# Kernel optimization log

Measured on AMD Instinct MI355X. Metric: run time of the kernel, lower is better.

The kernel has to match this reference:

```python
import jax, jax.numpy as jnp
import numpy as np
from jax import lax

B, T, D = 1024, 100, 12
NEG_SLOPE = 0.01  # torch.nn.LeakyReLU default


def setup_inputs() -> dict:
    key = jax.random.key(0)
    ks = jax.random.split(key, 6)
    y0 = jax.random.normal(ks[0], (B, T, D), dtype=jnp.float32)
    # shared, increasing time grid per row (forward only uses row 0, made relative)
    t = jnp.broadcast_to(jnp.linspace(0.0, 1.0, T, dtype=jnp.float32), (B, T)) + 0.0
    def lin(k, fan_in, fan_out):
        s = 1.0 / np.sqrt(fan_in)
        return jax.random.normal(k, (fan_in, fan_out), dtype=jnp.float32) * s
    W1 = lin(ks[1], D, 300); b1 = jnp.zeros((300,), jnp.float32)
    W2 = lin(ks[2], 300, 100); b2 = jnp.zeros((100,), jnp.float32)
    W3 = lin(ks[3], 100, 50); b3 = jnp.zeros((50,), jnp.float32)
    W4 = lin(ks[4], 50, D); b4 = jnp.zeros((D,), jnp.float32)
    return {"y0": y0, "t": t, "W1": W1, "b1": b1, "W2": W2, "b2": b2,
            "W3": W3, "b3": b3, "W4": W4, "b4": b4}


def _mlp(x, W1, b1, W2, b2, W3, b3, W4, b4):
    h = jax.nn.leaky_relu(x @ W1 + b1, NEG_SLOPE)
    h = jax.nn.leaky_relu(h @ W2 + b2, NEG_SLOPE)
    h = jax.nn.leaky_relu(h @ W3 + b3, NEG_SLOPE)
    return h @ W4 + b4


def reference(y0, t, W1, b1, W2, b2, W3, b3, W4, b4):
    # t_span: relative times of batch row 0 (as in the torch forward)
    t_rel = t[0] - t[0, 0]                       # [T]
    x0 = y0[:, 0, :]                             # [B, D] initial state
    f = lambda x: _mlp(x, W1, b1, W2, b2, W3, b3, W4, b4)

    def rk4_step(x, dt):
        k1 = f(x)
        k2 = f(x + 0.5 * dt * k1)
        k3 = f(x + 0.5 * dt * k2)
        k4 = f(x + dt * k3)
        x_new = x + (dt / 6.0) * (k1 + 2.0 * k2 + 2.0 * k3 + k4)
        return x_new, x_new

    dts = t_rel[1:] - t_rel[:-1]                 # [T-1]
    _, traj = lax.scan(rk4_step, x0, dts)        # [T-1, B, D]
    traj = jnp.concatenate([x0[None], traj], axis=0)  # [T, B, D]
    return jnp.swapaxes(traj, 0, 1)              # [B, T, D]
```

## Files before the change

kernel.cpp:

```cpp
#include <hip/hip_runtime.h>


typedef float v2f __attribute__((ext_vector_type(2)));
typedef float v4f __attribute__((ext_vector_type(4)));

constexpr int TT = 100;
constexpr int D  = 12;
constexpr int H1 = 300;
constexpr int H2 = 100;
constexpr int H3 = 50;
constexpr float NEG = 0.01f;

__device__ __forceinline__ float lrelu(float x) { return fmaxf(x, NEG * x); }
__device__ __forceinline__ v2f lo2(v4f v) { return __builtin_shufflevector(v, v, 0, 1); }
__device__ __forceinline__ v2f hi2(v4f v) { return __builtin_shufflevector(v, v, 2, 3); }
__device__ __forceinline__ v2f pkfma(v2f a, v2f b, v2f c) {
#if __has_builtin(__builtin_elementwise_fma)
    return __builtin_elementwise_fma(a, b, c);
#else
    return a * b + c;
#endif
}

__global__ __launch_bounds__(512)
void node_rk4_kernel(const float* __restrict__ y0, const float* __restrict__ t,
                     const float* __restrict__ W1, const float* __restrict__ b1,
                     const float* __restrict__ W2, const float* __restrict__ b2,
                     const float* __restrict__ W3, const float* __restrict__ b3,
                     const float* __restrict__ W4, const float* __restrict__ b4,
                     float* __restrict__ out)
{
    __shared__ __align__(16) float sW1 [D * H1];
    __shared__ __align__(16) float sW3c[25 * 200];
    __shared__ __align__(16) float sW4 [52 * 12];
    __shared__ __align__(16) float h1T [304 * 4];
    __shared__ __align__(16) float pL2 [32 * 104];
    __shared__ __align__(16) float h2e [4 * 104];
    __shared__ __align__(16) float h3e [4 * 52];
    __shared__ __align__(16) float sx  [48];
    __shared__ __align__(16) float sxe [48];
    __shared__ __align__(16) float sks [48];
    __shared__ float st [100];

    const int tid = threadIdx.x;
    const int l   = tid & 63;
    const int w   = tid >> 6;
    const bool l2act = (l < 50);

    const bool l1act = (tid < H1);
    const float rb1 = l1act ? b1[tid] : 0.0f;

    float w2a[38], w2b[38];
#pragma unroll
    for (int i = 0; i < 38; ++i) {
        const int k = w * 38 + i;
        float va = 0.0f, vb = 0.0f;
        if (l2act && k < H1) { va = W2[k * H2 + l]; vb = W2[k * H2 + l + 50]; }
        w2a[i] = va; w2b[i] = vb;
    }

    float rb2a = 0.f, rb2b = 0.f, rb3 = 0.f;
    if (w < 4 && l2act) { rb2a = b2[l]; rb2b = b2[l + 50]; rb3 = b3[l]; }

    const int u4 = tid - 256;
    const bool l4act = (u4 >= 0 && u4 < 192);
    int e4 = 0, j4 = 0, kq4 = 0;
    float b4v = 0.0f;
    if (l4act) {
        e4 = u4 / 48; const int r = u4 - e4 * 48; j4 = r >> 2; kq4 = r & 3;
        b4v = b4[j4];
    }

    for (int i = tid; i < D * H1; i += 512) sW1[i] = W1[i];
    for (int i = tid; i < H2 * H3; i += 512) {
        const int k = i / H3, j = i - k * H3;
        sW3c[(k >> 2) * 200 + j * 4 + (k & 3)] = W3[i];
    }
    for (int i = tid; i < 52 * 12; i += 512) sW4[i] = (i < H3 * D) ? W4[i] : 0.0f;
    if (tid < TT) st[tid] = t[tid];
    if (tid >= 104 && tid < 120) h1T[300 * 4 + (tid - 104)] = 0.0f;
    if (tid >= 120 && tid < 128) {
        const int u = tid - 120;
        h3e[(u >> 1) * 52 + 50 + (u & 1)] = 0.0f;
    }
    if (tid < 48) {
        const int e = tid / 12, j = tid - e * 12;
        const int g = (blockIdx.x * 4 + e) * (TT * D) + j;
        const float v = y0[g];
        sx[tid] = v;
        out[g]  = v;
    }
    __syncthreads();

    for (int s = 0; s < TT - 1; ++s) {
#pragma unroll 1
        for (int ev = 0; ev < 4; ++ev) {
            const float* xin = ev ? sxe : sx;

            if (l1act) {
                float wv[12];
#pragma unroll
                for (int k = 0; k < 12; ++k) wv[k] = sW1[k * H1 + tid];
                v4f r;
#pragma unroll
                for (int e = 0; e < 4; ++e) {
                    const v4f x0 = *(const v4f*)(xin + e * 12);
                    const v4f x1 = *(const v4f*)(xin + e * 12 + 4);
                    const v4f x2 = *(const v4f*)(xin + e * 12 + 8);
                    float a = rb1;
                    a = fmaf(x0.x, wv[0], a);  a = fmaf(x0.y, wv[1], a);
                    a = fmaf(x0.z, wv[2], a);  a = fmaf(x0.w, wv[3], a);
                    a = fmaf(x1.x, wv[4], a);  a = fmaf(x1.y, wv[5], a);
                    a = fmaf(x1.z, wv[6], a);  a = fmaf(x1.w, wv[7], a);
                    a = fmaf(x2.x, wv[8], a);  a = fmaf(x2.y, wv[9], a);
                    a = fmaf(x2.z, wv[10], a); a = fmaf(x2.w, wv[11], a);
                    r[e] = lrelu(a);
                }
                *(v4f*)(h1T + tid * 4) = r;
            }
            __syncthreads();

            {
                v2f a01A = {0,0}, a23A = {0,0}, a01B = {0,0}, a23B = {0,0};
                const float* hb = h1T + w * (38 * 4);
#pragma unroll
                for (int i = 0; i < 38; ++i) {
                    const v4f hv = *(const v4f*)(hb + i * 4);
                    const v2f wA = {w2a[i], w2a[i]};
                    const v2f wB = {w2b[i], w2b[i]};
                    a01A = pkfma(lo2(hv), wA, a01A);
                    a23A = pkfma(hi2(hv), wA, a23A);
                    a01B = pkfma(lo2(hv), wB, a01B);
                    a23B = pkfma(hi2(hv), wB, a23B);
                }
                if (l2act) {
                    pL2[(w * 4 + 0) * 104 + l]      = a01A.x;
                    pL2[(w * 4 + 1) * 104 + l]      = a01A.y;
                    pL2[(w * 4 + 2) * 104 + l]      = a23A.x;
                    pL2[(w * 4 + 3) * 104 + l]      = a23A.y;
                    pL2[(w * 4 + 0) * 104 + l + 50] = a01B.x;
                    pL2[(w * 4 + 1) * 104 + l + 50] = a01B.y;
                    pL2[(w * 4 + 2) * 104 + l + 50] = a23B.x;
                    pL2[(w * 4 + 3) * 104 + l + 50] = a23B.y;
                }
            }
            __syncthreads();

            if (w < 4 && l2act) {
                const int e = w;
                float va = rb2a, vb = rb2b;
#pragma unroll
                for (int q = 0; q < 8; ++q) {
                    va += pL2[(q * 4 + e) * 104 + l];
                    vb += pL2[(q * 4 + e) * 104 + l + 50];
                }
                h2e[e * 104 + l]      = lrelu(va);
                h2e[e * 104 + l + 50] = lrelu(vb);
                v2f acc = {0, 0};
                const float* hb2 = h2e + e * 104;
                const float* wb  = sW3c + l * 4;
#pragma unroll
                for (int c = 0; c < 25; ++c) {
                    const v4f wv = *(const v4f*)(wb + c * 200);
                    const v4f hv = *(const v4f*)(hb2 + c * 4);
                    acc = pkfma(lo2(hv), lo2(wv), acc);
                    acc = pkfma(hi2(hv), hi2(wv), acc);
                }
                h3e[e * 52 + l] = lrelu(acc.x + acc.y + rb3);
            }
            __syncthreads();

            if (l4act) {
                const int kb = kq4 * 13;
                float a = 0.0f;
                const float* hb3 = h3e + e4 * 52 + kb;
#pragma unroll
                for (int i = 0; i < 13; ++i)
                    a = fmaf(hb3[i], sW4[(kb + i) * 12 + j4], a);
                a += __shfl_xor(a, 1);
                a += __shfl_xor(a, 2);
                if (kq4 == 0) {
                    a += b4v;
                    const float dt = st[s + 1] - st[s];
                    const int bi = e4 * 12 + j4;
                    const float xc = sx[bi];
                    if (ev == 0)      { sks[bi] = a;        sxe[bi] = xc + 0.5f * dt * a; }
                    else if (ev == 1) { sks[bi] += 2.f * a; sxe[bi] = xc + 0.5f * dt * a; }
                    else if (ev == 2) { sks[bi] += 2.f * a; sxe[bi] = xc + dt * a; }
                    else {
                        const float xn = xc + dt * (1.0f / 6.0f) * (sks[bi] + a);
                        sx[bi] = xn;
                        out[(blockIdx.x * 4 + e4) * (TT * D) + (s + 1) * D + j4] = xn;
                    }
                }
            }
            __syncthreads();
        }
    }
}

extern "C" void kernel_launch(void* const* d_in, const int* in_sizes, int n_in,
                              void* d_out, int out_size, void* d_ws, size_t ws_size,
                              hipStream_t stream) {
    const float* y0 = (const float*)d_in[0];
    const float* t  = (const float*)d_in[1];
    const float* W1 = (const float*)d_in[2];
    const float* b1 = (const float*)d_in[3];
    const float* W2 = (const float*)d_in[4];
    const float* b2 = (const float*)d_in[5];
    const float* W3 = (const float*)d_in[6];
    const float* b3 = (const float*)d_in[7];
    const float* W4 = (const float*)d_in[8];
    const float* b4 = (const float*)d_in[9];
    float* out = (float*)d_out;

    node_rk4_kernel<<<256, 512, 0, stream>>>(y0, t, W1, b1, W2, b2, W3, b3, W4, b4, out);
}
```

Baseline: 1.170 ms.

## Fuse layers 3 and 4 per wave with readlane broadcasts, dropping a barrier

Layer 4 and the RK4 state update now run in the same four waves that compute layer 3, which removes one block-wide barrier per function evaluation. Layer 2 and layer 3 inputs are broadcast across lanes with readlane into scalar registers instead of being reread from LDS. The h2e buffer is gone. The RK4 state and accumulated slope live in registers rather than shared memory. In exchange there are many serial s_readlane instructions, with their latency and hazard stalls, and layers 3 and 4 are now serialised inside the same waves.

```diff
diff --git a/kernel.cpp b/kernel.cpp
--- a/kernel.cpp
+++ b/kernel.cpp
@@ -12,14 +12,8 @@
 constexpr float NEG = 0.01f;
 
 __device__ __forceinline__ float lrelu(float x) { return fmaxf(x, NEG * x); }
-__device__ __forceinline__ v2f lo2(v4f v) { return __builtin_shufflevector(v, v, 0, 1); }
-__device__ __forceinline__ v2f hi2(v4f v) { return __builtin_shufflevector(v, v, 2, 3); }
-__device__ __forceinline__ v2f pkfma(v2f a, v2f b, v2f c) {
-#if __has_builtin(__builtin_elementwise_fma)
-    return __builtin_elementwise_fma(a, b, c);
-#else
-    return a * b + c;
-#endif
+__device__ __forceinline__ float rdlane(float v, int lane) {
+    return __int_as_float(__builtin_amdgcn_readlane(__float_as_int(v), lane));
 }
 
 __global__ __launch_bounds__(512)
@@ -35,20 +29,16 @@
     __shared__ __align__(16) float sW4 [52 * 12];
     __shared__ __align__(16) float h1T [304 * 4];
     __shared__ __align__(16) float pL2 [32 * 104];
-    __shared__ __align__(16) float h2e [4 * 104];
     __shared__ __align__(16) float h3e [4 * 52];
     __shared__ __align__(16) float sx  [48];
     __shared__ __align__(16) float sxe [48];
-    __shared__ __align__(16) float sks [48];
     __shared__ float st [100];
 
     const int tid = threadIdx.x;
     const int l   = tid & 63;
     const int w   = tid >> 6;
     const bool l2act = (l < 50);
-
-    const bool l1act = (tid < H1);
-    const float rb1 = l1act ? b1[tid] : 0.0f;
+    const bool tw    = (w < 4);
 
     float w2a[38], w2b[38];
 #pragma unroll
@@ -59,17 +49,13 @@
         w2a[i] = va; w2b[i] = vb;
     }
 
+    const bool l1act = (tid < H1);
+    const float rb1 = l1act ? b1[tid] : 0.0f;
+
     float rb2a = 0.f, rb2b = 0.f, rb3 = 0.f;
-    if (w < 4 && l2act) { rb2a = b2[l]; rb2b = b2[l + 50]; rb3 = b3[l]; }
-
-    const int u4 = tid - 256;
-    const bool l4act = (u4 >= 0 && u4 < 192);
-    int e4 = 0, j4 = 0, kq4 = 0;
-    float b4v = 0.0f;
-    if (l4act) {
-        e4 = u4 / 48; const int r = u4 - e4 * 48; j4 = r >> 2; kq4 = r & 3;
-        b4v = b4[j4];
-    }
+    if (tw && l2act) { rb2a = b2[l]; rb2b = b2[l + 50]; rb3 = b3[l]; }
+    const int j4 = l >> 2, kq4 = l & 3;
+    const float b4v = (tw && l < 48) ? b4[j4] : 0.0f;
 
     for (int i = tid; i < D * H1; i += 512) sW1[i] = W1[i];
     for (int i = tid; i < H2 * H3; i += 512) {
@@ -92,7 +78,11 @@
     }
     __syncthreads();
 
+    float xreg = 0.0f, ks = 0.0f;
+    if (tw && l < 48 && kq4 == 0) xreg = sx[w * 12 + j4];
+
     for (int s = 0; s < TT - 1; ++s) {
+        const float dt = st[s + 1] - st[s];
 #pragma unroll 1
         for (int ev = 0; ev < 4; ++ev) {
             const float* xin = ev ? sxe : sx;
@@ -121,76 +111,79 @@
             __syncthreads();
 
             {
-                v2f a01A = {0,0}, a23A = {0,0}, a01B = {0,0}, a23B = {0,0};
-                const float* hb = h1T + w * (38 * 4);
+                const int ksrc = w * 38 + ((l < 38) ? l : 37);
+                const v4f hv = *(const v4f*)(h1T + ksrc * 4);
+                float a0A = 0.f, a0B = 0.f, a1A = 0.f, a1B = 0.f;
+                float a2A = 0.f, a2B = 0.f, a3A = 0.f, a3B = 0.f;
 #pragma unroll
                 for (int i = 0; i < 38; ++i) {
-                    const v4f hv = *(const v4f*)(hb + i * 4);
-                    const v2f wA = {w2a[i], w2a[i]};
-                    const v2f wB = {w2b[i], w2b[i]};
-                    a01A = pkfma(lo2(hv), wA, a01A);
-                    a23A = pkfma(hi2(hv), wA, a23A);
-                    a01B = pkfma(lo2(hv), wB, a01B);
-                    a23B = pkfma(hi2(hv), wB, a23B);
+                    const float h0 = rdlane(hv[0], i);
+                    const float h1 = rdlane(hv[1], i);
+                    const float h2 = rdlane(hv[2], i);
+                    const float h3 = rdlane(hv[3], i);
+                    a0A = fmaf(h0, w2a[i], a0A);  a0B = fmaf(h0, w2b[i], a0B);
+                    a1A = fmaf(h1, w2a[i], a1A);  a1B = fmaf(h1, w2b[i], a1B);
+                    a2A = fmaf(h2, w2a[i], a2A);  a2B = fmaf(h2, w2b[i], a2B);
+                    a3A = fmaf(h3, w2a[i], a3A);  a3B = fmaf(h3, w2b[i], a3B);
                 }
                 if (l2act) {
-                    pL2[(w * 4 + 0) * 104 + l]      = a01A.x;
-                    pL2[(w * 4 + 1) * 104 + l]      = a01A.y;
-                    pL2[(w * 4 + 2) * 104 + l]      = a23A.x;
-                    pL2[(w * 4 + 3) * 104 + l]      = a23A.y;
-                    pL2[(w * 4 + 0) * 104 + l + 50] = a01B.x;
-                    pL2[(w * 4 + 1) * 104 + l + 50] = a01B.y;
-                    pL2[(w * 4 + 2) * 104 + l + 50] = a23B.x;
-                    pL2[(w * 4 + 3) * 104 + l + 50] = a23B.y;
+                    pL2[(w * 4 + 0) * 104 + l]      = a0A;
+                    pL2[(w * 4 + 1) * 104 + l]      = a1A;
+                    pL2[(w * 4 + 2) * 104 + l]      = a2A;
+                    pL2[(w * 4 + 3) * 104 + l]      = a3A;
+                    pL2[(w * 4 + 0) * 104 + l + 50] = a0B;
+                    pL2[(w * 4 + 1) * 104 + l + 50] = a1B;
+                    pL2[(w * 4 + 2) * 104 + l + 50] = a2B;
+                    pL2[(w * 4 + 3) * 104 + l + 50] = a3B;
                 }
             }
             __syncthreads();
 
-            if (w < 4 && l2act) {
+            if (tw) {
                 const int e = w;
-                float va = rb2a, vb = rb2b;
-#pragma unroll
-                for (int q = 0; q < 8; ++q) {
-                    va += pL2[(q * 4 + e) * 104 + l];
-                    vb += pL2[(q * 4 + e) * 104 + l + 50];
-                }
-                h2e[e * 104 + l]      = lrelu(va);
-                h2e[e * 104 + l + 50] = lrelu(vb);
-                v2f acc = {0, 0};
-                const float* hb2 = h2e + e * 104;
-                const float* wb  = sW3c + l * 4;
-#pragma unroll
-                for (int c = 0; c < 25; ++c) {
-                    const v4f wv = *(const v4f*)(wb + c * 200);
-                    const v4f hv = *(const v4f*)(hb2 + c * 4);
-                    acc = pkfma(lo2(hv), lo2(wv), acc);
-                    acc = pkfma(hi2(hv), hi2(wv), acc);
-                }
-                h3e[e * 52 + l] = lrelu(acc.x + acc.y + rb3);
-            }
-            __syncthreads();
-
-            if (l4act) {
-                const int kb = kq4 * 13;
-                float a = 0.0f;
-                const float* hb3 = h3e + e4 * 52 + kb;
-#pragma unroll
-                for (int i = 0; i < 13; ++i)
-                    a = fmaf(hb3[i], sW4[(kb + i) * 12 + j4], a);
-                a += __shfl_xor(a, 1);
-                a += __shfl_xor(a, 2);
-                if (kq4 == 0) {
-                    a += b4v;
-                    const float dt = st[s + 1] - st[s];
-                    const int bi = e4 * 12 + j4;
-                    const float xc = sx[bi];
-                    if (ev == 0)      { sks[bi] = a;        sxe[bi] = xc + 0.5f * dt * a; }
-                    else if (ev == 1) { sks[bi] += 2.f * a; sxe[bi] = xc + 0.5f * dt * a; }
-                    else if (ev == 2) { sks[bi] += 2.f * a; sxe[bi] = xc + dt * a; }
-                    else {
-                        const float xn = xc + dt * (1.0f / 6.0f) * (sks[bi] + a);
-                        sx[bi] = xn;
-                        out[(blockIdx.x * 4 + e4) * (TT * D) + (s + 1) * D + j4] = xn;
+                if (l2act) {
+                    float va = rb2a, vb = rb2b;
+#pragma unroll
+                    for (int q = 0; q < 8; ++q) {
+                        va += pL2[(q * 4 + e) * 104 + l];
+                        vb += pL2[(q * 4 + e) * 104 + l + 50];
+                    }
+                    const float h2a = lrelu(va);
+                    const float h2b = lrelu(vb);
+                    float acc = rb3;
+#pragma unroll
+                    for (int c = 0; c < 25; ++c) {
+                        const v4f wv = *(const v4f*)(sW3c + c * 200 + l * 4);
+#pragma unroll
+                        for (int q = 0; q < 4; ++q) {
+                            const int kk = 4 * c + q;
+                            const float h = (kk < 50) ? rdlane(h2a, kk)
+                                                      : rdlane(h2b, kk - 50);
+                            acc = fmaf(h, wv[q], acc);
+                        }
+                    }
+                    h3e[e * 52 + l] = lrelu(acc);
+                }
+                if (l < 48) {
+                    const int kb = kq4 * 13;
+                    float a = 0.0f;
+#pragma unroll
+                    for (int i = 0; i < 13; ++i)
+                        a = fmaf(h3e[e * 52 + kb + i], sW4[(kb + i) * 12 + j4], a);
+                    a += __shfl_xor(a, 1);
+                    a += __shfl_xor(a, 2);
+                    if (kq4 == 0) {
+                        a += b4v;
+                        const int bi = e * 12 + j4;
+                        if (ev == 0)      { ks = a;          sxe[bi] = xreg + 0.5f * dt * a; }
+                        else if (ev == 1) { ks += 2.f * a;   sxe[bi] = xreg + 0.5f * dt * a; }
+                        else if (ev == 2) { ks += 2.f * a;   sxe[bi] = xreg + dt * a; }
+                        else {
+                            const float xn = xreg + dt * (1.0f / 6.0f) * (ks + a);
+                            xreg = xn;
+                            sx[bi] = xn;
+                            out[(blockIdx.x * 4 + e) * (TT * D) + (s + 1) * D + j4] = xn;
+                        }
                     }
                 }
             }
```

After: 1.641 ms. +40.2%, slower.
